# Kernel tuning notes

Measured on AMD Instinct MI355X. Metric: run time of the kernel, lower is better.

## Reference

```python
import jax, jax.numpy as jnp
import numpy as np

STRIDE = 1
PADDING = 0


def setup_inputs() -> dict:
    key = jax.random.key(0)
    k1, k2, k3 = jax.random.split(key, 3)
    B, E, Cin, Cout, H, W = 32, 8, 64, 64, 160, 160
    x = jax.random.normal(k1, (B, Cin, H, W), dtype=jnp.float32)
    alpha = jax.random.uniform(k2, (B, E), dtype=jnp.float32)
    kernel_embed = jax.random.normal(k3, (E, Cout, Cin, 1, 1), dtype=jnp.float32)
    return {"x": x, "alpha": alpha, "kernel_embed": kernel_embed}


def reference(x, alpha, kernel_embed):
    # Per-sample kernel mix: [B,E] x [E,O,I,kh,kw] -> [B,O,I,kh,kw]
    kernels = jnp.einsum('be,eoihw->boihw', alpha, kernel_embed)

    def conv_one(xi, ki):
        # xi: [Cin,H,W], ki: [Cout,Cin,kh,kw]
        out = jax.lax.conv_general_dilated(
            xi[None],  # [1,Cin,H,W]
            ki,
            window_strides=(STRIDE, STRIDE),
            padding=[(PADDING, PADDING), (PADDING, PADDING)],
            dimension_numbers=('NCHW', 'OIHW', 'NCHW'),
        )
        return out[0]  # [Cout,Ho,Wo]

    return jax.vmap(conv_one)(x, kernels)  # [B,Cout,Ho,Wo]
```

## Files before the change

### kernel.cpp

```cpp
#include <hip/hip_runtime.h>
#include <cstdint>
#include <cstddef>


#define PIX 25600
#define CIN 64
#define COUT 64
#define BATCH 32
#define NEXP 8
#define TILE_PX 256
#define TILES_PER_B (PIX / TILE_PX)

__device__ __forceinline__ void load_lds16(const float* g, float* l) {
  __builtin_amdgcn_global_load_lds(
      (__attribute__((address_space(1))) void*)(g),
      (__attribute__((address_space(3))) void*)(l), 16, 0, 0);
}

__global__ __launch_bounds__(256) void mix_kernel(
    const float* __restrict__ alpha, const float* __restrict__ ke,
    float* __restrict__ kt) {
  const int b = blockIdx.x >> 3;
  const int seg = blockIdx.x & 7;
  __shared__ float a[NEXP];
  if (threadIdx.x < NEXP) a[threadIdx.x] = alpha[b * NEXP + threadIdx.x];
  __syncthreads();
#pragma unroll
  for (int t = 0; t < 2; t++) {
    const int idx = seg * 512 + t * 256 + threadIdx.x;
    float s = 0.f;
#pragma unroll
    for (int e = 0; e < NEXP; e++) s += a[e] * ke[e * 4096 + idx];
    const int o = idx >> 6, i = idx & 63;
    kt[b * 4096 + i * 64 + o] = s;
  }
}

__global__ __launch_bounds__(256, 3) void conv_kernel(
    const float* __restrict__ x, const float* __restrict__ kt,
    float* __restrict__ out) {
  __shared__ float ks[CIN * COUT];
  __shared__ float xs[32 * TILE_PX];

  const int bid = blockIdx.x;
  const int b = bid / TILES_PER_B;
  const int tile = bid - b * TILES_PER_B;
  const int P0 = tile * TILE_PX;

  const int tid = threadIdx.x;
  const int wave = tid >> 6;
  const int lane = tid & 63;
  const int tc = tid >> 5;
  const int tp = tid & 31;

  const float* xb = x + (size_t)b * CIN * PIX + P0;
  const float* kb = kt + b * 4096;

#pragma unroll
  for (int j = 0; j < 4; j++) {
    const int row = wave * 4 + j;
    load_lds16(kb + row * 256 + lane * 4, &ks[row * 256]);
  }

  const int swzl = lane ^ ((lane >> 3) & 7);

#pragma unroll
  for (int j = 0; j < 8; j++) {
    const int i = wave * 8 + j;
    load_lds16(xb + (size_t)i * PIX + swzl * 4, &xs[i * TILE_PX]);
  }

  float acc[8][8];
#pragma unroll
  for (int c = 0; c < 8; c++)
#pragma unroll
    for (int p = 0; p < 8; p++) acc[c][p] = 0.f;

  const int g0 = 2 * tp, g1 = 2 * tp + 1;
  const int off0 = (g0 ^ ((g0 >> 3) & 7)) * 16;
  const int off1 = (g1 ^ ((g1 >> 3) & 7)) * 16;
  const char* xsb = (const char*)xs;
  const int kcol = tc * 8;

  __syncthreads();

#pragma unroll 2
  for (int ii = 0; ii < 32; ii++) {
    const float4 xv0 = *(const float4*)(xsb + ii * (TILE_PX * 4) + off0);
    const float4 xv1 = *(const float4*)(xsb + ii * (TILE_PX * 4) + off1);
    const float4 k0 = *(const float4*)&ks[ii * 64 + kcol];
    const float4 k1 = *(const float4*)&ks[ii * 64 + kcol + 4];
    const float kc[8] = {k0.x, k0.y, k0.z, k0.w, k1.x, k1.y, k1.z, k1.w};
    const float xp[8] = {xv0.x, xv0.y, xv0.z, xv0.w, xv1.x, xv1.y, xv1.z, xv1.w};
#pragma unroll
    for (int c = 0; c < 8; c++)
#pragma unroll
      for (int p = 0; p < 8; p++) acc[c][p] = fmaf(kc[c], xp[p], acc[c][p]);
  }

  __syncthreads();

#pragma unroll
  for (int j = 0; j < 8; j++) {
    const int i = 32 + wave * 8 + j;
    load_lds16(xb + (size_t)i * PIX + swzl * 4, &xs[(i - 32) * TILE_PX]);
  }

  __syncthreads();

#pragma unroll 2
  for (int ii = 0; ii < 32; ii++) {
    const float4 xv0 = *(const float4*)(xsb + ii * (TILE_PX * 4) + off0);
    const float4 xv1 = *(const float4*)(xsb + ii * (TILE_PX * 4) + off1);
    const float4 k0 = *(const float4*)&ks[(32 + ii) * 64 + kcol];
    const float4 k1 = *(const float4*)&ks[(32 + ii) * 64 + kcol + 4];
    const float kc[8] = {k0.x, k0.y, k0.z, k0.w, k1.x, k1.y, k1.z, k1.w};
    const float xp[8] = {xv0.x, xv0.y, xv0.z, xv0.w, xv1.x, xv1.y, xv1.z, xv1.w};
#pragma unroll
    for (int c = 0; c < 8; c++)
#pragma unroll
      for (int p = 0; p < 8; p++) acc[c][p] = fmaf(kc[c], xp[p], acc[c][p]);
  }

  float* ob = out + ((size_t)(b * COUT + tc * 8)) * PIX + P0 + tp * 8;
#pragma unroll
  for (int c = 0; c < 8; c++) {
    *(float4*)(ob + (size_t)c * PIX) =
        make_float4(acc[c][0], acc[c][1], acc[c][2], acc[c][3]);
    *(float4*)(ob + (size_t)c * PIX + 4) =
        make_float4(acc[c][4], acc[c][5], acc[c][6], acc[c][7]);
  }
}

extern "C" void kernel_launch(void* const* d_in, const int* in_sizes, int n_in,
                              void* d_out, int out_size, void* d_ws,
                              size_t ws_size, hipStream_t stream) {
  const float* x = (const float*)d_in[0];
  const float* alpha = (const float*)d_in[1];
  const float* ke = (const float*)d_in[2];
  float* out = (float*)d_out;
  float* kt = (float*)d_ws;

  mix_kernel<<<BATCH * 8, 256, 0, stream>>>(alpha, ke, kt);
  conv_kernel<<<BATCH * TILES_PER_B, 256, 0, stream>>>(x, kt, out);
}
```

Before: 362.2 us.

## Halve pixel tile and load all input channels in a single stage

Shrinks the conv tile from 256 to 128 pixels and gives each thread an 8x4 accumulator block instead of 8x8. All 64 input channels are staged into LDS at once, which removes the two-phase reload with its extra barriers and drops the XOR swizzle. The aim is more blocks and waves in flight with fewer registers, to better hide memory latency in this bandwidth-bound conv. The cost is lower arithmetic intensity per LDS load, twice as many kernel-tile reloads per pixel, and possible LDS bank conflicts without the swizzle.

```diff
diff --git a/kernel.cpp b/kernel.cpp
--- a/kernel.cpp
+++ b/kernel.cpp
@@ -8,7 +8,7 @@
 #define COUT 64
 #define BATCH 32
 #define NEXP 8
-#define TILE_PX 256
+#define TILE_PX 128
 #define TILES_PER_B (PIX / TILE_PX)
 
 __device__ __forceinline__ void load_lds16(const float* g, float* l) {
@@ -40,7 +40,7 @@
     const float* __restrict__ x, const float* __restrict__ kt,
     float* __restrict__ out) {
   __shared__ float ks[CIN * COUT];
-  __shared__ float xs[32 * TILE_PX];
+  __shared__ float xs[CIN * TILE_PX];
 
   const int bid = blockIdx.x;
   const int b = bid / TILES_PER_B;
@@ -58,77 +58,45 @@
 
 #pragma unroll
   for (int j = 0; j < 4; j++) {
-    const int row = wave * 4 + j;
-    load_lds16(kb + row * 256 + lane * 4, &ks[row * 256]);
+    const int r = wave * 4 + j;
+    load_lds16(kb + r * 256 + lane * 4, &ks[r * 256]);
   }
-
-  const int swzl = lane ^ ((lane >> 3) & 7);
 
 #pragma unroll
   for (int j = 0; j < 8; j++) {
-    const int i = wave * 8 + j;
-    load_lds16(xb + (size_t)i * PIX + swzl * 4, &xs[i * TILE_PX]);
+    const int r = wave * 16 + j * 2;
+    load_lds16(xb + (size_t)(r + (lane >> 5)) * PIX + (lane & 31) * 4,
+               &xs[r * TILE_PX]);
   }
 
-  float acc[8][8];
+  float acc[8][4];
 #pragma unroll
   for (int c = 0; c < 8; c++)
 #pragma unroll
-    for (int p = 0; p < 8; p++) acc[c][p] = 0.f;
-
-  const int g0 = 2 * tp, g1 = 2 * tp + 1;
-  const int off0 = (g0 ^ ((g0 >> 3) & 7)) * 16;
-  const int off1 = (g1 ^ ((g1 >> 3) & 7)) * 16;
-  const char* xsb = (const char*)xs;
-  const int kcol = tc * 8;
+    for (int p = 0; p < 4; p++) acc[c][p] = 0.f;
 
   __syncthreads();
 
-#pragma unroll 2
-  for (int ii = 0; ii < 32; ii++) {
-    const float4 xv0 = *(const float4*)(xsb + ii * (TILE_PX * 4) + off0);
-    const float4 xv1 = *(const float4*)(xsb + ii * (TILE_PX * 4) + off1);
-    const float4 k0 = *(const float4*)&ks[ii * 64 + kcol];
-    const float4 k1 = *(const float4*)&ks[ii * 64 + kcol + 4];
+  const float* xp4 = xs + tp * 4;
+  const float* kp = ks + tc * 8;
+#pragma unroll 8
+  for (int ii = 0; ii < CIN; ii++) {
+    const float4 xv = *(const float4*)(xp4 + ii * TILE_PX);
+    const float4 k0 = *(const float4*)(kp + ii * 64);
+    const float4 k1 = *(const float4*)(kp + ii * 64 + 4);
     const float kc[8] = {k0.x, k0.y, k0.z, k0.w, k1.x, k1.y, k1.z, k1.w};
-    const float xp[8] = {xv0.x, xv0.y, xv0.z, xv0.w, xv1.x, xv1.y, xv1.z, xv1.w};
+    const float xv4[4] = {xv.x, xv.y, xv.z, xv.w};
 #pragma unroll
     for (int c = 0; c < 8; c++)
 #pragma unroll
-      for (int p = 0; p < 8; p++) acc[c][p] = fmaf(kc[c], xp[p], acc[c][p]);
+      for (int p = 0; p < 4; p++) acc[c][p] = fmaf(kc[c], xv4[p], acc[c][p]);
   }
 
-  __syncthreads();
-
-#pragma unroll
-  for (int j = 0; j < 8; j++) {
-    const int i = 32 + wave * 8 + j;
-    load_lds16(xb + (size_t)i * PIX + swzl * 4, &xs[(i - 32) * TILE_PX]);
-  }
-
-  __syncthreads();
-
-#pragma unroll 2
-  for (int ii = 0; ii < 32; ii++) {
-    const float4 xv0 = *(const float4*)(xsb + ii * (TILE_PX * 4) + off0);
-    const float4 xv1 = *(const float4*)(xsb + ii * (TILE_PX * 4) + off1);
-    const float4 k0 = *(const float4*)&ks[(32 + ii) * 64 + kcol];
-    const float4 k1 = *(const float4*)&ks[(32 + ii) * 64 + kcol + 4];
-    const float kc[8] = {k0.x, k0.y, k0.z, k0.w, k1.x, k1.y, k1.z, k1.w};
-    const float xp[8] = {xv0.x, xv0.y, xv0.z, xv0.w, xv1.x, xv1.y, xv1.z, xv1.w};
-#pragma unroll
-    for (int c = 0; c < 8; c++)
-#pragma unroll
-      for (int p = 0; p < 8; p++) acc[c][p] = fmaf(kc[c], xp[p], acc[c][p]);
-  }
-
-  float* ob = out + ((size_t)(b * COUT + tc * 8)) * PIX + P0 + tp * 8;
+  float* ob = out + ((size_t)(b * COUT + tc * 8)) * PIX + P0 + tp * 4;
 #pragma unroll
   for (int c = 0; c < 8; c++) {
     *(float4*)(ob + (size_t)c * PIX) =
         make_float4(acc[c][0], acc[c][1], acc[c][2], acc[c][3]);
-    *(float4*)(ob + (size_t)c * PIX + 4) =
-        make_float4(acc[c][4], acc[c][5], acc[c][6], acc[c][7]);
   }
 }
 
```

Measured after the change: 353.8 us. 2.3% less time.
